# Kernel tuning notes

Hardware: AMD Instinct MI355X
Metric: run time of the kernel (lower is better)

Reference implementation:

```python
import jax, jax.numpy as jnp
import numpy as np

N, DEG, C_IN, C_OUT, T, HID, EPS = 20000, 16, 128, 128, 3, 128, 0.01
MLP_IN = C_IN * (1 + T)


def setup_inputs() -> dict:
    key = jax.random.key(0)
    ks = jax.random.split(key, 14)
    node_attr = jax.random.normal(ks[0], (N, C_IN), jnp.float32)
    # uniform-degree graph: edges sorted by source node (CSR layout)
    src = jnp.repeat(jnp.arange(N, dtype=jnp.int32), DEG)
    dst = jax.random.randint(ks[1], (N * DEG,), 0, N, dtype=jnp.int32)
    edge_index = jnp.stack([src, dst], axis=0)
    slices = jnp.stack([jnp.arange(N, dtype=jnp.int32) * DEG,
                        jnp.full((N,), DEG, jnp.int32)], axis=1)
    s1 = 1.0 / np.sqrt(MLP_IN)
    s2 = 1.0 / np.sqrt(64)
    sg = 1.0 / np.sqrt(HID)
    W1 = jax.random.uniform(ks[2], (MLP_IN, 64), jnp.float32, -s1, s1)
    b1 = jnp.zeros((64,), jnp.float32)
    W2 = jax.random.uniform(ks[3], (64, 1), jnp.float32, -s2, s2)
    b2 = jnp.zeros((1,), jnp.float32)
    Wih = jax.random.uniform(ks[4], (3 * HID, C_IN), jnp.float32, -sg, sg)
    Whh = jax.random.uniform(ks[5], (3 * HID, HID), jnp.float32, -sg, sg)
    bih = jax.random.uniform(ks[6], (3 * HID,), jnp.float32, -sg, sg)
    bhh = jax.random.uniform(ks[7], (3 * HID,), jnp.float32, -sg, sg)
    Wout = jax.random.uniform(ks[8], (HID, C_OUT), jnp.float32, -sg, sg)
    bout = jnp.zeros((C_OUT,), jnp.float32)
    # pre-sampled selection noise (torch.randn per step in the original)
    noise = jax.random.normal(ks[9], (T, N, DEG), jnp.float32)
    return {"node_attr": node_attr, "edge_index": edge_index, "slices": slices,
            "W1": W1, "b1": b1, "W2": W2, "b2": b2,
            "Wih": Wih, "Whh": Whh, "bih": bih, "bhh": bhh,
            "Wout": Wout, "bout": bout, "noise": noise}


def _forward(node_attr, edge_index, W1, b1, W2, b2, Wih, Whh, bih, bhh, Wout, bout, noise):
    v = node_attr
    num_nodes, c = v.shape
    deg = edge_index.shape[1] // num_nodes
    nbr = edge_index[1].reshape(num_nodes, deg)  # uniform-degree CSR neighbors

    walks_last = jnp.arange(num_nodes)
    walk_embeds = jnp.zeros((num_nodes, 1 + T, c), v.dtype).at[:, 0, :].set(v)

    for t in range(T):  # small fixed walk length
        cand = nbr[walks_last]                                   # [N, deg]
        v_t = v[cand]                                            # [N, deg, c]
        we_t = jnp.broadcast_to(walk_embeds[:, None], (num_nodes, deg, 1 + T, c))
        we_t = we_t.at[:, :, 1 + t, :].set(v_t)                  # candidate walk embeds
        flat = we_t.reshape(num_nodes, deg, (1 + T) * c)
        h = jax.nn.relu(flat @ W1 + b1)                          # tiny scoring MLP
        logp = (h @ W2 + b2)[..., 0]                             # [N, deg]
        logp = jax.lax.stop_gradient(logp)                       # torch.no_grad in original
        norm = jax.nn.logsumexp(logp, axis=1, keepdims=True)     # scatter_logsumexp per node
        walk_p = jnp.exp(logp - norm) + EPS * noise[t]
        sel = jnp.argmax(walk_p, axis=1)                         # noisy scatter_max per node
        walks_t = jnp.take_along_axis(cand, sel[:, None], axis=1)[:, 0]
        walk_embeds = walk_embeds.at[:, 1 + t, :].set(v[walks_t])
        walks_last = walks_t

    # GRUAggr: 1-layer GRU (hidden 128) over the walk sequence, then Linear -> C_OUT
    seq = jnp.transpose(walk_embeds, (1, 0, 2))  # [1+T, N, c]

    def gru_step(hprev, x):
        gi = x @ Wih.T + bih
        gh = hprev @ Whh.T + bhh
        ir, iz, inn = jnp.split(gi, 3, axis=-1)
        hr, hz, hn = jnp.split(gh, 3, axis=-1)
        r = jax.nn.sigmoid(ir + hr)
        z = jax.nn.sigmoid(iz + hz)
        n = jnp.tanh(inn + r * hn)
        hnew = (1.0 - z) * n + z * hprev
        return hnew, None

    h0 = jnp.zeros((num_nodes, HID), v.dtype)
    h_last, _ = jax.lax.scan(gru_step, h0, seq)
    return h_last @ Wout + bout  # [N, C_OUT]


def reference(node_attr, edge_index, slices, W1, b1, W2, b2, Wih, Whh, bih, bhh, Wout, bout, noise):
    del slices  # uniform degree encoded directly in edge_index layout
    return _forward(node_attr, edge_index, W1, b1, W2, b2, Wih, Whh, bih, bhh, Wout, bout, noise)
```

## Files before the change

kernel.cpp:

```cpp
#include <hip/hip_runtime.h>
#include <hip/hip_bf16.h>
#include <math.h>

#define NN 20000
#define DEGV 16
#define CINV 128
#define TSTEPS 3
#define HIDV 128

typedef float f32x4 __attribute__((ext_vector_type(4)));
typedef short s16x8 __attribute__((ext_vector_type(8)));

#define MFMA16(a, b, c) __builtin_amdgcn_mfma_f32_16x16x32_bf16(a, b, c, 0, 0, 0)

static __device__ __forceinline__ short f2bf(float x) {
    __hip_bfloat16 h = __float2bfloat16(x);
    return *reinterpret_cast<short*>(&h);
}

__global__ __launch_bounds__(256) void k_precompute(
    const float* __restrict__ v, const float* __restrict__ W1,
    const float* __restrict__ b1,
    float* __restrict__ P, float* __restrict__ base, int* __restrict__ walk_idx,
    short* __restrict__ vb)
{
    __shared__ float vt[32][129];
    int nb = blockIdx.x * 32;
    for (int idx = threadIdx.x; idx < 32 * 128; idx += 256) {
        int nl = idx >> 7, k = idx & 127;
        float x = v[(size_t)(nb + nl) * 128 + k];
        vt[nl][k] = x;
        vb[(size_t)(nb + nl) * 128 + k] = f2bf(x);
    }
    __syncthreads();

    int s  = threadIdx.x >> 6;
    int jg = (threadIdx.x >> 2) & 15;
    int ng = threadIdx.x & 3;

    double accd[8][4];
#pragma unroll
    for (int i = 0; i < 8; ++i)
#pragma unroll
        for (int m = 0; m < 4; ++m) accd[i][m] = 0.0;

    const float* w1s = W1 + (size_t)s * 128 * 64 + jg;

    for (int kb = 0; kb < 8; ++kb) {
        float acc[8][4];
#pragma unroll
        for (int i = 0; i < 8; ++i)
#pragma unroll
            for (int m = 0; m < 4; ++m) acc[i][m] = 0.f;
#pragma unroll
        for (int kk = 0; kk < 16; ++kk) {
            int k = kb * 16 + kk;
            float w0 = w1s[k * 64 +  0];
            float w1 = w1s[k * 64 + 16];
            float w2 = w1s[k * 64 + 32];
            float w3 = w1s[k * 64 + 48];
#pragma unroll
            for (int i = 0; i < 8; ++i) {
                float xv = vt[ng * 8 + i][k];
                acc[i][0] = fmaf(xv, w0, acc[i][0]);
                acc[i][1] = fmaf(xv, w1, acc[i][1]);
                acc[i][2] = fmaf(xv, w2, acc[i][2]);
                acc[i][3] = fmaf(xv, w3, acc[i][3]);
            }
        }
#pragma unroll
        for (int i = 0; i < 8; ++i)
#pragma unroll
            for (int m = 0; m < 4; ++m) accd[i][m] += (double)acc[i][m];
    }

#pragma unroll
    for (int i = 0; i < 8; ++i) {
        int n = nb + ng * 8 + i;
#pragma unroll
        for (int m = 0; m < 4; ++m) {
            int j = jg + 16 * m;
            float pv = (float)accd[i][m];
            P[(size_t)s * NN * 64 + (size_t)n * 64 + j] = pv;
            if (s == 0) {
                base[(size_t)n * 64 + j] = pv + b1[j];
                if (j == 0) walk_idx[n] = n;
            }
        }
    }
}

__global__ __launch_bounds__(256) void k_walk_step(
    const float* __restrict__ P, float* __restrict__ base,
    const int* __restrict__ dst, const float* __restrict__ W2,
    const float* __restrict__ b2, const float* __restrict__ noise,
    int* __restrict__ walk_idx, int t)
{
    int wave = threadIdx.x >> 6;
    int lane = threadIdx.x & 63;
    int n = blockIdx.x * 4 + wave;
    if (n >= NN) return;

    int wl = walk_idx[t * NN + n];
    int d = lane >> 2, sub = lane & 3;
    int cand = dst[wl * DEGV + d];

    const float* Pslice = P + (size_t)(t + 1) * NN * 64;
    const float4* b4 = (const float4*)(base + (size_t)n * 64);
    const float4* p4 = (const float4*)(Pslice + (size_t)cand * 64);
    const float4* w4 = (const float4*)W2;

    double acc = 0.0;
#pragma unroll
    for (int k = 0; k < 4; ++k) {
        float4 bb = b4[sub * 4 + k];
        float4 pp = p4[sub * 4 + k];
        float4 ww = w4[sub * 4 + k];
        acc += (double)fmaxf(bb.x + pp.x, 0.f) * (double)ww.x;
        acc += (double)fmaxf(bb.y + pp.y, 0.f) * (double)ww.y;
        acc += (double)fmaxf(bb.z + pp.z, 0.f) * (double)ww.z;
        acc += (double)fmaxf(bb.w + pp.w, 0.f) * (double)ww.w;
    }
    acc += __shfl_xor(acc, 1);
    acc += __shfl_xor(acc, 2);
    double logp = acc + (double)b2[0];

    double m = logp;
    for (int mask = 4; mask < 64; mask <<= 1) m = fmax(m, __shfl_xor(m, mask));
    double e = exp(logp - m);
    double ssum = e;
    for (int mask = 4; mask < 64; mask <<= 1) ssum += __shfl_xor(ssum, mask);
    double norm = m + log(ssum);

    double wp = exp(logp - norm) +
                0.01 * (double)noise[((size_t)t * NN + n) * DEGV + d];

    int bd = d;
    double bwp = wp;
    for (int mask = 4; mask < 64; mask <<= 1) {
        double owp = __shfl_xor(bwp, mask);
        int od = __shfl_xor(bd, mask);
        if (owp > bwp || (owp == bwp && od < bd)) { bwp = owp; bd = od; }
    }
    int sel = dst[wl * DEGV + bd];

    base[(size_t)n * 64 + lane] += Pslice[(size_t)sel * 64 + lane];
    if (lane == 0) walk_idx[(t + 1) * NN + n] = sel;
}

__global__ __launch_bounds__(256) void k_convert_w(
    const float* __restrict__ Wih, const float* __restrict__ Whh,
    const float* __restrict__ Wout,
    short* __restrict__ Wihb, short* __restrict__ Whhb, short* __restrict__ WoutTb)
{
    int idx = blockIdx.x * 256 + threadIdx.x;
    if (idx < 49152) {
        Wihb[idx] = f2bf(Wih[idx]);
    } else if (idx < 98304) {
        int e = idx - 49152;
        Whhb[e] = f2bf(Whh[e]);
    } else if (idx < 114688) {
        int e = idx - 98304;
        int o = e >> 7, k = e & 127;
        WoutTb[e] = f2bf(Wout[k * 128 + o]);
    }
}

__global__ __launch_bounds__(512, 2) void k_gru_fused(
    const short* __restrict__ vb, const int* __restrict__ widx,
    const short* __restrict__ Wihb, const short* __restrict__ Whhb,
    const short* __restrict__ WoutTb,
    const float* __restrict__ bih, const float* __restrict__ bhh,
    const float* __restrict__ bout, float* __restrict__ out)
{
    __shared__ short x_bf[2][32][136];
    __shared__ short h_bf[32][136];
    int tid = threadIdx.x;
    int j = tid >> 6, lane = tid & 63;
    int c = lane & 15, q = lane >> 4;
    int nb = blockIdx.x * 32;
    int u = j * 16 + c;

    float b_r  = bih[u] + bhh[u];
    float b_z  = bih[128 + u] + bhh[128 + u];
    float b_in = bih[256 + u];
    float b_hn = bhh[256 + u];

    const short* bi_base = Wihb   + c * 128 + q * 8 + j * 2048;
    const short* bh_base = Whhb   + c * 128 + q * 8 + j * 2048;
    const short* bo_base = WoutTb + c * 128 + q * 8 + j * 2048;

    s16x8 wiR[4], wiZ[4], wiN[4], whR[4], whZ[4], whN[4], wo[4];
#pragma unroll
    for (int ks = 0; ks < 4; ++ks) {
        wiR[ks] = *(const s16x8*)(bi_base + ks * 32);
        wiZ[ks] = *(const s16x8*)(bi_base + 8 * 2048 + ks * 32);
        wiN[ks] = *(const s16x8*)(bi_base + 16 * 2048 + ks * 32);
        whR[ks] = *(const s16x8*)(bh_base + ks * 32);
        whZ[ks] = *(const s16x8*)(bh_base + 8 * 2048 + ks * 32);
        whN[ks] = *(const s16x8*)(bh_base + 16 * 2048 + ks * 32);
        wo[ks]  = *(const s16x8*)(bo_base + ks * 32);
    }

    float h_reg[2][4];
#pragma unroll
    for (int g = 0; g < 2; ++g)
#pragma unroll
        for (int i = 0; i < 4; ++i) h_reg[g][i] = 0.f;

    int srow = tid >> 4, schunk = tid & 15;

    {
        int src = widx[nb + srow];
        *(s16x8*)&x_bf[0][srow][schunk * 8] =
            *(const s16x8*)(vb + (size_t)src * 128 + schunk * 8);
    }
    __syncthreads();

#pragma unroll 1
    for (int t = 0; t < 1 + TSTEPS; ++t) {
        int cur = t & 1;

        s16x8 pref;
        if (t < TSTEPS) {
            int src = widx[(t + 1) * NN + nb + srow];
            pref = *(const s16x8*)(vb + (size_t)src * 128 + schunk * 8);
        }

        float rr[2][4], zz[2][4];

        {
            f32x4 zf = {0.f, 0.f, 0.f, 0.f};
            f32x4 aR[2] = {zf, zf}, aZ[2] = {zf, zf};
#pragma unroll
            for (int ks = 0; ks < 4; ++ks) {
#pragma unroll
                for (int g = 0; g < 2; ++g) {
                    s16x8 a = *(const s16x8*)&x_bf[cur][g * 16 + c][ks * 32 + q * 8];
                    aR[g] = MFMA16(a, wiR[ks], aR[g]);
                    aZ[g] = MFMA16(a, wiZ[ks], aZ[g]);
                }
            }
            if (t > 0) {
#pragma unroll
                for (int ks = 0; ks < 4; ++ks) {
#pragma unroll
                    for (int g = 0; g < 2; ++g) {
                        s16x8 a = *(const s16x8*)&h_bf[g * 16 + c][ks * 32 + q * 8];
                        aR[g] = MFMA16(a, whR[ks], aR[g]);
                        aZ[g] = MFMA16(a, whZ[ks], aZ[g]);
                    }
                }
            }
#pragma unroll
            for (int g = 0; g < 2; ++g)
#pragma unroll
                for (int i = 0; i < 4; ++i) {
                    rr[g][i] = 1.f / (1.f + __expf(-(aR[g][i] + b_r)));
                    zz[g][i] = 1.f / (1.f + __expf(-(aZ[g][i] + b_z)));
                }
        }

        {
            f32x4 zf = {0.f, 0.f, 0.f, 0.f};
            f32x4 aIN[2] = {zf, zf}, aHN[2] = {zf, zf};
#pragma unroll
            for (int ks = 0; ks < 4; ++ks) {
#pragma unroll
                for (int g = 0; g < 2; ++g) {
                    s16x8 a = *(const s16x8*)&x_bf[cur][g * 16 + c][ks * 32 + q * 8];
                    aIN[g] = MFMA16(a, wiN[ks], aIN[g]);
                }
            }
            if (t > 0) {
#pragma unroll
                for (int ks = 0; ks < 4; ++ks) {
#pragma unroll
                    for (int g = 0; g < 2; ++g) {
                        s16x8 a = *(const s16x8*)&h_bf[g * 16 + c][ks * 32 + q * 8];
                        aHN[g] = MFMA16(a, whN[ks], aHN[g]);
                    }
                }
            }
            __syncthreads();
            if (t < TSTEPS)
                *(s16x8*)&x_bf[cur ^ 1][srow][schunk * 8] = pref;
#pragma unroll
            for (int g = 0; g < 2; ++g)
#pragma unroll
                for (int i = 0; i < 4; ++i) {
                    float narg = aIN[g][i] + b_in + rr[g][i] * (aHN[g][i] + b_hn);
                    float e2 = __expf(2.f * narg);
                    float ngt = 1.f - 2.f / (e2 + 1.f);
                    float hn = (1.f - zz[g][i]) * ngt + zz[g][i] * h_reg[g][i];
                    h_reg[g][i] = hn;
                    h_bf[g * 16 + q * 4 + i][u] = f2bf(hn);
                }
        }
        __syncthreads();
    }

    {
        f32x4 zf = {0.f, 0.f, 0.f, 0.f};
        f32x4 acco[2] = {zf, zf};
#pragma unroll
        for (int ks = 0; ks < 4; ++ks) {
#pragma unroll
            for (int g = 0; g < 2; ++g) {
                s16x8 a = *(const s16x8*)&h_bf[g * 16 + c][ks * 32 + q * 8];
                acco[g] = MFMA16(a, wo[ks], acco[g]);
            }
        }
        float bb = bout[u];
#pragma unroll
        for (int g = 0; g < 2; ++g)
#pragma unroll
            for (int i = 0; i < 4; ++i)
                out[(size_t)(nb + g * 16 + q * 4 + i) * 128 + u] = acco[g][i] + bb;
    }
}

extern "C" void kernel_launch(void* const* d_in, const int* in_sizes, int n_in,
                              void* d_out, int out_size, void* d_ws, size_t ws_size,
                              hipStream_t stream)
{
    const float* node_attr = (const float*)d_in[0];
    const int*   edge_index = (const int*)d_in[1];
    const float* W1  = (const float*)d_in[3];
    const float* b1  = (const float*)d_in[4];
    const float* W2  = (const float*)d_in[5];
    const float* b2  = (const float*)d_in[6];
    const float* Wih = (const float*)d_in[7];
    const float* Whh = (const float*)d_in[8];
    const float* bih = (const float*)d_in[9];
    const float* bhh = (const float*)d_in[10];
    const float* Wout = (const float*)d_in[11];
    const float* bout = (const float*)d_in[12];
    const float* noise = (const float*)d_in[13];

    const int* dst = edge_index + (size_t)NN * DEGV;

    char* ws = (char*)d_ws;
    size_t offP    = 0;
    size_t offBase = offP + (size_t)4 * NN * 64 * 4;
    size_t offW    = offBase + (size_t)NN * 64 * 4;
    size_t offWidx = offW + (size_t)(2 * 49152 + 16384) * 2;
    size_t offVb   = offWidx + (size_t)4 * NN * 4;
    float* P    = (float*)(ws + offP);
    float* base = (float*)(ws + offBase);
    short* Wihb   = (short*)(ws + offW);
    short* Whhb   = Wihb + 384 * 128;
    short* WoutTb = Whhb + 384 * 128;
    int*   widx = (int*)(ws + offWidx);
    short* vb   = (short*)(ws + offVb);

    dim3 blk(256);
    k_convert_w<<<dim3(448), blk, 0, stream>>>(Wih, Whh, Wout, Wihb, Whhb, WoutTb);
    k_precompute<<<dim3(625), blk, 0, stream>>>(node_attr, W1, b1, P, base, widx, vb);
    for (int t = 0; t < TSTEPS; ++t)
        k_walk_step<<<dim3(5000), blk, 0, stream>>>(P, base, dst, W2, b2, noise, widx, t);
    k_gru_fused<<<dim3(625), dim3(512), 0, stream>>>(vb, widx, Wihb, Whhb, WoutTb,
                                                     bih, bhh, bout, (float*)d_out);
}
```

Measured before the change: 168.5 us.

## Halve GRU tile to 16 nodes per block and vectorize swizzled precompute LDS reads

The fused GRU kernel now processes 16 nodes per block instead of 32, doubling the grid to 1250 blocks. Each step computes all gate MFMAs from a single load of x and h fragments into registers, and only half the threads stage the next walk's inputs. The precompute kernel switches its LDS tile to an XOR-swizzled layout so each thread can read float4 vectors and avoid bank conflicts. The smaller tile improves occupancy and load balance, at the cost of loading weights into registers twice as often across blocks and leaving half the staging threads idle.

```diff
diff --git a/kernel.cpp b/kernel.cpp
--- a/kernel.cpp
+++ b/kernel.cpp
@@ -24,12 +24,13 @@
     float* __restrict__ P, float* __restrict__ base, int* __restrict__ walk_idx,
     short* __restrict__ vb)
 {
-    __shared__ float vt[32][129];
+    __shared__ float vt[32][132];
     int nb = blockIdx.x * 32;
     for (int idx = threadIdx.x; idx < 32 * 128; idx += 256) {
         int nl = idx >> 7, k = idx & 127;
         float x = v[(size_t)(nb + nl) * 128 + k];
-        vt[nl][k] = x;
+        int k4 = (k >> 2) ^ (nl >> 3);
+        vt[nl][(k4 << 2) | (k & 3)] = x;
         vb[(size_t)(nb + nl) * 128 + k] = f2bf(x);
     }
     __syncthreads();
@@ -53,19 +54,28 @@
 #pragma unroll
             for (int m = 0; m < 4; ++m) acc[i][m] = 0.f;
 #pragma unroll
-        for (int kk = 0; kk < 16; ++kk) {
-            int k = kb * 16 + kk;
-            float w0 = w1s[k * 64 +  0];
-            float w1 = w1s[k * 64 + 16];
-            float w2 = w1s[k * 64 + 32];
-            float w3 = w1s[k * 64 + 48];
-#pragma unroll
-            for (int i = 0; i < 8; ++i) {
-                float xv = vt[ng * 8 + i][k];
-                acc[i][0] = fmaf(xv, w0, acc[i][0]);
-                acc[i][1] = fmaf(xv, w1, acc[i][1]);
-                acc[i][2] = fmaf(xv, w2, acc[i][2]);
-                acc[i][3] = fmaf(xv, w3, acc[i][3]);
+        for (int kq = 0; kq < 4; ++kq) {
+            int K4 = kb * 4 + kq;
+            float4 xv[8];
+#pragma unroll
+            for (int i = 0; i < 8; ++i)
+                xv[i] = *(const float4*)&vt[ng * 8 + i][(K4 ^ ng) << 2];
+#pragma unroll
+            for (int kk = 0; kk < 4; ++kk) {
+                int k = K4 * 4 + kk;
+                float w0 = w1s[k * 64 +  0];
+                float w1 = w1s[k * 64 + 16];
+                float w2 = w1s[k * 64 + 32];
+                float w3 = w1s[k * 64 + 48];
+#pragma unroll
+                for (int i = 0; i < 8; ++i) {
+                    float x = (kk == 0) ? xv[i].x : (kk == 1) ? xv[i].y
+                            : (kk == 2) ? xv[i].z : xv[i].w;
+                    acc[i][0] = fmaf(x, w0, acc[i][0]);
+                    acc[i][1] = fmaf(x, w1, acc[i][1]);
+                    acc[i][2] = fmaf(x, w2, acc[i][2]);
+                    acc[i][3] = fmaf(x, w3, acc[i][3]);
+                }
             }
         }
 #pragma unroll
@@ -173,12 +183,12 @@
     const float* __restrict__ bih, const float* __restrict__ bhh,
     const float* __restrict__ bout, float* __restrict__ out)
 {
-    __shared__ short x_bf[2][32][136];
-    __shared__ short h_bf[32][136];
+    __shared__ short x_bf[2][16][136];
+    __shared__ short h_bf[16][136];
     int tid = threadIdx.x;
     int j = tid >> 6, lane = tid & 63;
     int c = lane & 15, q = lane >> 4;
-    int nb = blockIdx.x * 32;
+    int nb = blockIdx.x * 16;
     int u = j * 16 + c;
 
     float b_r  = bih[u] + bhh[u];
@@ -202,15 +212,14 @@
         wo[ks]  = *(const s16x8*)(bo_base + ks * 32);
     }
 
-    float h_reg[2][4];
-#pragma unroll
-    for (int g = 0; g < 2; ++g)
-#pragma unroll
-        for (int i = 0; i < 4; ++i) h_reg[g][i] = 0.f;
+    float h_reg[4];
+#pragma unroll
+    for (int i = 0; i < 4; ++i) h_reg[i] = 0.f;
 
     int srow = tid >> 4, schunk = tid & 15;
-
-    {
+    bool stager = srow < 16;
+
+    if (stager) {
         int src = widx[nb + srow];
         *(s16x8*)&x_bf[0][srow][schunk * 8] =
             *(const s16x8*)(vb + (size_t)src * 128 + schunk * 8);
@@ -222,101 +231,70 @@
         int cur = t & 1;
 
         s16x8 pref;
-        if (t < TSTEPS) {
+        if (t < TSTEPS && stager) {
             int src = widx[(t + 1) * NN + nb + srow];
             pref = *(const s16x8*)(vb + (size_t)src * 128 + schunk * 8);
         }
 
-        float rr[2][4], zz[2][4];
-
-        {
-            f32x4 zf = {0.f, 0.f, 0.f, 0.f};
-            f32x4 aR[2] = {zf, zf}, aZ[2] = {zf, zf};
+        s16x8 ax[4], ah[4];
+#pragma unroll
+        for (int ks = 0; ks < 4; ++ks)
+            ax[ks] = *(const s16x8*)&x_bf[cur][c][ks * 32 + q * 8];
+        if (t > 0) {
+#pragma unroll
+            for (int ks = 0; ks < 4; ++ks)
+                ah[ks] = *(const s16x8*)&h_bf[c][ks * 32 + q * 8];
+        }
+
+        f32x4 zf = {0.f, 0.f, 0.f, 0.f};
+        f32x4 aR = zf, aZ = zf, aIN = zf, aHN = zf;
+#pragma unroll
+        for (int ks = 0; ks < 4; ++ks) {
+            aR  = MFMA16(ax[ks], wiR[ks], aR);
+            aZ  = MFMA16(ax[ks], wiZ[ks], aZ);
+            aIN = MFMA16(ax[ks], wiN[ks], aIN);
+        }
+        if (t > 0) {
 #pragma unroll
             for (int ks = 0; ks < 4; ++ks) {
-#pragma unroll
-                for (int g = 0; g < 2; ++g) {
-                    s16x8 a = *(const s16x8*)&x_bf[cur][g * 16 + c][ks * 32 + q * 8];
-                    aR[g] = MFMA16(a, wiR[ks], aR[g]);
-                    aZ[g] = MFMA16(a, wiZ[ks], aZ[g]);
-                }
+                aR  = MFMA16(ah[ks], whR[ks], aR);
+                aZ  = MFMA16(ah[ks], whZ[ks], aZ);
+                aHN = MFMA16(ah[ks], whN[ks], aHN);
             }
-            if (t > 0) {
-#pragma unroll
-                for (int ks = 0; ks < 4; ++ks) {
-#pragma unroll
-                    for (int g = 0; g < 2; ++g) {
-                        s16x8 a = *(const s16x8*)&h_bf[g * 16 + c][ks * 32 + q * 8];
-                        aR[g] = MFMA16(a, whR[ks], aR[g]);
-                        aZ[g] = MFMA16(a, whZ[ks], aZ[g]);
-                    }
-                }
-            }
-#pragma unroll
-            for (int g = 0; g < 2; ++g)
-#pragma unroll
-                for (int i = 0; i < 4; ++i) {
-                    rr[g][i] = 1.f / (1.f + __expf(-(aR[g][i] + b_r)));
-                    zz[g][i] = 1.f / (1.f + __expf(-(aZ[g][i] + b_z)));
-                }
-        }
-
-        {
-            f32x4 zf = {0.f, 0.f, 0.f, 0.f};
-            f32x4 aIN[2] = {zf, zf}, aHN[2] = {zf, zf};
-#pragma unroll
-            for (int ks = 0; ks < 4; ++ks) {
-#pragma unroll
-                for (int g = 0; g < 2; ++g) {
-                    s16x8 a = *(const s16x8*)&x_bf[cur][g * 16 + c][ks * 32 + q * 8];
-                    aIN[g] = MFMA16(a, wiN[ks], aIN[g]);
-                }
-            }
-            if (t > 0) {
-#pragma unroll
-                for (int ks = 0; ks < 4; ++ks) {
-#pragma unroll
-                    for (int g = 0; g < 2; ++g) {
-                        s16x8 a = *(const s16x8*)&h_bf[g * 16 + c][ks * 32 + q * 8];
-                        aHN[g] = MFMA16(a, whN[ks], aHN[g]);
-                    }
-                }
-            }
-            __syncthreads();
-            if (t < TSTEPS)
-                *(s16x8*)&x_bf[cur ^ 1][srow][schunk * 8] = pref;
-#pragma unroll
-            for (int g = 0; g < 2; ++g)
-#pragma unroll
-                for (int i = 0; i < 4; ++i) {
-                    float narg = aIN[g][i] + b_in + rr[g][i] * (aHN[g][i] + b_hn);
-                    float e2 = __expf(2.f * narg);
-                    float ngt = 1.f - 2.f / (e2 + 1.f);
-                    float hn = (1.f - zz[g][i]) * ngt + zz[g][i] * h_reg[g][i];
-                    h_reg[g][i] = hn;
-                    h_bf[g * 16 + q * 4 + i][u] = f2bf(hn);
-                }
-        }
+        }
+
         __syncthreads();
+        if (t < TSTEPS && stager)
+            *(s16x8*)&x_bf[cur ^ 1][srow][schunk * 8] = pref;
+
+#pragma unroll
+        for (int i = 0; i < 4; ++i) {
+            float r = 1.f / (1.f + __expf(-(aR[i] + b_r)));
+            float z = 1.f / (1.f + __expf(-(aZ[i] + b_z)));
+            float hnarg = (t > 0) ? (aHN[i] + b_hn) : b_hn;
+            float narg = aIN[i] + b_in + r * hnarg;
+            float e2 = __expf(2.f * narg);
+            float ngt = 1.f - 2.f / (e2 + 1.f);
+            float hn = (1.f - z) * ngt + z * h_reg[i];
+            h_reg[i] = hn;
+            h_bf[q * 4 + i][u] = f2bf(hn);
+        }
+        __syncthreads();
     }
 
     {
-        f32x4 zf = {0.f, 0.f, 0.f, 0.f};
-        f32x4 acco[2] = {zf, zf};
-#pragma unroll
-        for (int ks = 0; ks < 4; ++ks) {
-#pragma unroll
-            for (int g = 0; g < 2; ++g) {
-                s16x8 a = *(const s16x8*)&h_bf[g * 16 + c][ks * 32 + q * 8];
-                acco[g] = MFMA16(a, wo[ks], acco[g]);
-            }
-        }
+        s16x8 ah2[4];
+#pragma unroll
+        for (int ks = 0; ks < 4; ++ks)
+            ah2[ks] = *(const s16x8*)&h_bf[c][ks * 32 + q * 8];
+        f32x4 acco = {0.f, 0.f, 0.f, 0.f};
+#pragma unroll
+        for (int ks = 0; ks < 4; ++ks)
+            acco = MFMA16(ah2[ks], wo[ks], acco);
         float bb = bout[u];
 #pragma unroll
-        for (int g = 0; g < 2; ++g)
-#pragma unroll
-            for (int i = 0; i < 4; ++i)
-                out[(size_t)(nb + g * 16 + q * 4 + i) * 128 + u] = acco[g][i] + bb;
+        for (int i = 0; i < 4; ++i)
+            out[(size_t)(nb + q * 4 + i) * 128 + u] = acco[i] + bb;
     }
 }
 
@@ -359,6 +337,6 @@
     k_precompute<<<dim3(625), blk, 0, stream>>>(node_attr, W1, b1, P, base, widx, vb);
     for (int t = 0; t < TSTEPS; ++t)
         k_walk_step<<<dim3(5000), blk, 0, stream>>>(P, base, dst, W2, b2, noise, widx, t);
-    k_gru_fused<<<dim3(625), dim3(512), 0, stream>>>(vb, widx, Wihb, Whhb, WoutTb,
-                                                     bih, bhh, bout, (float*)d_out);
-}
+    k_gru_fused<<<dim3(1250), dim3(512), 0, stream>>>(vb, widx, Wihb, Whhb, WoutTb,
+                                                      bih, bhh, bout, (float*)d_out);
+}
```

Result: slower. 175.4 us (+4.1%).
